# Performance work log

Measured on AMD Instinct MI355X. Metric: run time of the kernel, lower is better.

Reference implementation:

```python
import jax, jax.numpy as jnp
import numpy as np

D_EMB = 1024
N_H = 16
D_H = D_EMB // N_H

def setup_inputs() -> dict:
    key = jax.random.key(0)
    ks = jax.random.split(key, 9)
    s = 1.0 / np.sqrt(D_EMB)
    inp = {"x": jax.random.normal(ks[0], (2, 2048, D_EMB), dtype=jnp.float32)}
    for i, name in enumerate(["q", "k", "v", "o"]):
        inp[f"W{name}"] = jax.random.uniform(ks[1 + 2 * i], (D_EMB, D_EMB), minval=-s, maxval=s, dtype=jnp.float32)
        inp[f"b{name}"] = jax.random.uniform(ks[2 + 2 * i], (D_EMB,), minval=-s, maxval=s, dtype=jnp.float32)
    return inp

def reference(x, Wq, bq, Wk, bk, Wv, bv, Wo, bo):
    B, S, D = x.shape
    # torch Linear: y = x @ W.T + b
    Q = x @ Wq.T + bq
    K = x @ Wk.T + bk
    V = x @ Wv.T + bv
    # [B, H, S, d_h]
    Qh = Q.reshape(B, S, N_H, D_H).transpose(0, 2, 1, 3)
    Kh = K.reshape(B, S, N_H, D_H).transpose(0, 2, 1, 3)
    Vh = V.reshape(B, S, N_H, D_H).transpose(0, 2, 1, 3)
    scores = jnp.einsum("bhsd,bhtd->bhst", Qh, Kh) / jnp.sqrt(jnp.float32(D_H))
    causal = jnp.tril(jnp.ones((S, S), dtype=bool))
    scores = jnp.where(causal, scores, -jnp.inf)
    attn = jax.nn.softmax(scores, axis=-1)
    out = jnp.einsum("bhst,bhtd->bhsd", attn, Vh)
    out = out.transpose(0, 2, 1, 3).reshape(B, S, D)
    return out @ Wo.T + bo
```

## Files before the change

kernel.cpp:

```cpp
#include <hip/hip_runtime.h>
#include <stdint.h>

#define B_  2
#define S_  2048
#define D_  1024
#define H_  16
#define DH_ 64
#define M_  (B_ * S_)

#define NEG_BIG   (-1.0e30f)
#define EXP_FLOOR (-60.0f)
#define FIXED_M   16.0f

typedef uint16_t u16;
typedef uint32_t u32;
typedef u16   u16x4  __attribute__((ext_vector_type(4)));
typedef u16   u16x8  __attribute__((ext_vector_type(8)));
typedef u32   u32x4  __attribute__((ext_vector_type(4)));
typedef __bf16 bf16_t;
typedef bf16_t bf16x8 __attribute__((ext_vector_type(8)));
typedef float floatx4 __attribute__((ext_vector_type(4)));

__device__ __forceinline__ u16 f2b(float f) {
  u32 u = __float_as_uint(f);
  return (u16)((u + 0x7FFFu + ((u >> 16) & 1u)) >> 16);
}
__device__ __forceinline__ u16x8 tr8(const float* p) {
  u16x8 lo = *(const u16x8*)p;
  u16x8 hi = *(const u16x8*)(p + 4);
  return __builtin_shufflevector(lo, hi, 1, 3, 5, 7, 9, 11, 13, 15);
}
__device__ __forceinline__ bf16x8 bc8(u16x8 v) { return __builtin_bit_cast(bf16x8, v); }

__global__ __launch_bounds__(256) void qkv_kernel(
    const float* __restrict__ X,
    const float* __restrict__ Wq, const float* __restrict__ Wk, const float* __restrict__ Wv,
    const float* __restrict__ bq, const float* __restrict__ bk, const float* __restrict__ bv,
    u16* __restrict__ Qb, u16* __restrict__ Kb, u16* __restrict__ Vb)
{
  const int which = blockIdx.y >> 3;
  const float* W    = (which == 0) ? Wq : (which == 1) ? Wk : Wv;
  const float* bias = (which == 0) ? bq : (which == 1) ? bk : bv;
  u16* Y            = (which == 0) ? Qb : (which == 1) ? Kb : Vb;
  const int gm = blockIdx.x * 128;
  const int gn = (blockIdx.y & 7) * 128;

  __shared__ u16 Xl[128][40];
  __shared__ u16 Wl[128][40];

  const int t    = threadIdx.x;
  const int srow = t >> 1;
  const int scol = (t & 1) * 16;
  const int wave = t >> 6;
  const int lane = t & 63;
  const int wm = (wave >> 1) * 64, wn = (wave & 1) * 64;
  const int c = lane & 15, g = lane >> 4;

  const float* xsrc = X + (size_t)(gm + srow) * D_ + scol;
  const float* wsrc = W + (size_t)(gn + srow) * D_ + scol;

  u16x8 xr0 = tr8(xsrc), xr1 = tr8(xsrc + 8);
  u16x8 wr0 = tr8(wsrc), wr1 = tr8(wsrc + 8);

  floatx4 acc[4][4] = {};

  for (int kb = 0; kb < D_; kb += 32) {
    __syncthreads();
    *(u16x8*)&Xl[srow][scol]     = xr0;
    *(u16x8*)&Xl[srow][scol + 8] = xr1;
    *(u16x8*)&Wl[srow][scol]     = wr0;
    *(u16x8*)&Wl[srow][scol + 8] = wr1;
    __syncthreads();

    if (kb + 32 < D_) {
      xr0 = tr8(xsrc + kb + 32); xr1 = tr8(xsrc + kb + 40);
      wr0 = tr8(wsrc + kb + 32); wr1 = tr8(wsrc + kb + 40);
    }

    bf16x8 am[4], bn[4];
#pragma unroll
    for (int i = 0; i < 4; ++i) {
      am[i] = bc8(*(const u16x8*)&Xl[wm + 16 * i + c][8 * g]);
      bn[i] = bc8(*(const u16x8*)&Wl[wn + 16 * i + c][8 * g]);
    }
#pragma unroll
    for (int mi = 0; mi < 4; ++mi)
#pragma unroll
      for (int ni = 0; ni < 4; ++ni)
        acc[mi][ni] = __builtin_amdgcn_mfma_f32_16x16x32_bf16(am[mi], bn[ni], acc[mi][ni], 0, 0, 0);
  }

#pragma unroll
  for (int ni = 0; ni < 4; ++ni) {
    const int col = gn + wn + 16 * ni + c;
    const float bv_ = bias[col];
#pragma unroll
    for (int mi = 0; mi < 4; ++mi)
#pragma unroll
      for (int r = 0; r < 4; ++r)
        Y[(size_t)(gm + wm + 16 * mi + 4 * g + r) * D_ + col] = f2b(acc[mi][ni][r] + bv_);
  }
}

__global__ __launch_bounds__(256) void proj_kernel(
    const u16* __restrict__ A, const float* __restrict__ W,
    const float* __restrict__ bias, float* __restrict__ Y)
{
  const int gm = blockIdx.x * 128;
  const int gn = blockIdx.y * 64;

  __shared__ u16 Al[128][40];
  __shared__ u16 Wl[64][40];

  const int t = threadIdx.x;
  const int wave = t >> 6, lane = t & 63;
  const int wm = (wave >> 1) * 64, wn = (wave & 1) * 32;
  const int c = lane & 15, g = lane >> 4;
  const int ar_ = t >> 1, ac_ = (t & 1) * 16;
  const int wr_ = t >> 2, wc_ = (t & 3) * 8;

  const u16*   asrc = A + (size_t)(gm + ar_) * D_ + ac_;
  const float* wsrc = W + (size_t)(gn + wr_) * D_ + wc_;

  u16x8 a0 = *(const u16x8*)asrc;
  u16x8 a1 = *(const u16x8*)(asrc + 8);
  u16x8 w0 = tr8(wsrc);

  floatx4 acc[4][2] = {};

  for (int kb = 0; kb < D_; kb += 32) {
    __syncthreads();
    *(u16x8*)&Al[ar_][ac_]     = a0;
    *(u16x8*)&Al[ar_][ac_ + 8] = a1;
    *(u16x8*)&Wl[wr_][wc_]     = w0;
    __syncthreads();

    if (kb + 32 < D_) {
      a0 = *(const u16x8*)(asrc + kb + 32);
      a1 = *(const u16x8*)(asrc + kb + 40);
      w0 = tr8(wsrc + kb + 32);
    }

    bf16x8 am[4], bn[2];
#pragma unroll
    for (int i = 0; i < 4; ++i) am[i] = bc8(*(const u16x8*)&Al[wm + 16 * i + c][8 * g]);
#pragma unroll
    for (int i = 0; i < 2; ++i) bn[i] = bc8(*(const u16x8*)&Wl[wn + 16 * i + c][8 * g]);
#pragma unroll
    for (int mi = 0; mi < 4; ++mi)
#pragma unroll
      for (int ni = 0; ni < 2; ++ni)
        acc[mi][ni] = __builtin_amdgcn_mfma_f32_16x16x32_bf16(am[mi], bn[ni], acc[mi][ni], 0, 0, 0);
  }

#pragma unroll
  for (int ni = 0; ni < 2; ++ni) {
    const int col = gn + wn + 16 * ni + c;
    const float bv_ = bias[col];
#pragma unroll
    for (int mi = 0; mi < 4; ++mi)
#pragma unroll
      for (int r = 0; r < 4; ++r)
        Y[(size_t)(gm + wm + 16 * mi + 4 * g + r) * D_ + col] = acc[mi][ni][r] + bv_;
  }
}

__global__ __launch_bounds__(256) void attn_kernel(
    const u16* __restrict__ Qg, const u16* __restrict__ Kg,
    const u16* __restrict__ Vg, u16* __restrict__ Og)
{
  const int bh = blockIdx.x;
  const int b = bh >> 4, h = bh & 15;
  const int qb = 31 - blockIdx.y;
  const int q0 = qb * 64;

  __shared__ u16 Kl[64][72];
  __shared__ u16 Vt[64][72];

  const int t = threadIdx.x;
  const int wave = t >> 6, lane = t & 63;
  const int c = lane & 15, g = lane >> 4;
  const int qrow = q0 + wave * 16 + c;

  bf16x8 qf[2];
  {
    const u16* qsrc = Qg + (size_t)(b * S_ + qrow) * D_ + h * DH_ + 8 * g;
    qf[0] = bc8(*(const u16x8*)qsrc);
    qf[1] = bc8(*(const u16x8*)(qsrc + 32));
  }

  float l_run = 0.f;
  floatx4 o[4] = {};

  const int kr = t >> 2, kc = (t & 3) * 16;
  const int vkp = t & 31, vdg = t >> 5;

  u16x8 kreg0, kreg1;
  u32 vpack[8];
  {
    const u16* ksrc = Kg + (size_t)(b * S_ + kr) * D_ + h * DH_ + kc;
    kreg0 = *(const u16x8*)ksrc;
    kreg1 = *(const u16x8*)(ksrc + 8);
    const u16* vsrc = Vg + (size_t)(b * S_ + 2 * vkp) * D_ + h * DH_ + 8 * vdg;
    u16x8 va = *(const u16x8*)vsrc;
    u16x8 vb2 = *(const u16x8*)(vsrc + D_);
#pragma unroll
    for (int i = 0; i < 8; ++i) vpack[i] = (u32)va[i] | ((u32)vb2[i] << 16);
  }

  for (int kt = 0; kt <= qb; ++kt) {
    const int k0 = kt * 64;
    __syncthreads();
    *(u16x8*)&Kl[kr][kc]     = kreg0;
    *(u16x8*)&Kl[kr][kc + 8] = kreg1;
#pragma unroll
    for (int i = 0; i < 8; ++i) *(u32*)&Vt[8 * vdg + i][2 * vkp] = vpack[i];
    __syncthreads();

    if (kt < qb) {
      const u16* ksrc = Kg + (size_t)(b * S_ + k0 + 64 + kr) * D_ + h * DH_ + kc;
      kreg0 = *(const u16x8*)ksrc;
      kreg1 = *(const u16x8*)(ksrc + 8);
      const u16* vsrc = Vg + (size_t)(b * S_ + k0 + 64 + 2 * vkp) * D_ + h * DH_ + 8 * vdg;
      u16x8 va = *(const u16x8*)vsrc;
      u16x8 vb2 = *(const u16x8*)(vsrc + D_);
#pragma unroll
      for (int i = 0; i < 8; ++i) vpack[i] = (u32)va[i] | ((u32)vb2[i] << 16);
    }

    floatx4 st[4] = {};
#pragma unroll
    for (int mb = 0; mb < 4; ++mb) {
      bf16x8 a0 = bc8(*(const u16x8*)&Kl[16 * mb + c][8 * g]);
      bf16x8 a1 = bc8(*(const u16x8*)&Kl[16 * mb + c][32 + 8 * g]);
      st[mb] = __builtin_amdgcn_mfma_f32_16x16x32_bf16(a0, qf[0], st[mb], 0, 0, 0);
      st[mb] = __builtin_amdgcn_mfma_f32_16x16x32_bf16(a1, qf[1], st[mb], 0, 0, 0);
    }

    u32 plo[4], phi[4];
    float psum = 0.f;
    const bool diag = (kt == qb);
#pragma unroll
    for (int mb = 0; mb < 4; ++mb) {
      u32 pb[4];
#pragma unroll
      for (int r = 0; r < 4; ++r) {
        float arg = fmaf(st[mb][r], 0.125f, -FIXED_M);
        if (diag && (k0 + 16 * mb + 4 * g + r > qrow)) arg = NEG_BIG;
        arg = fmaxf(arg, EXP_FLOOR);
        float p = __expf(arg);
        pb[r] = __float_as_uint(p) & 0xFFFF0000u;
        psum += __uint_as_float(pb[r]);
      }
      plo[mb] = (pb[0] >> 16) | pb[1];
      phi[mb] = (pb[2] >> 16) | pb[3];
    }
    l_run += psum;

    const int s1 = c + 32 * (g & 1);
    const int s2 = s1 + 16;
    const bool hi = (g >= 2);
#pragma unroll
    for (int ks = 0; ks < 2; ++ks) {
      u32 q0a = (u32)__shfl((int)plo[2 * ks],     s1);
      u32 q1a = (u32)__shfl((int)phi[2 * ks],     s1);
      u32 q2a = (u32)__shfl((int)plo[2 * ks],     s2);
      u32 q3a = (u32)__shfl((int)phi[2 * ks],     s2);
      u32 q0b = (u32)__shfl((int)plo[2 * ks + 1], s1);
      u32 q1b = (u32)__shfl((int)phi[2 * ks + 1], s1);
      u32 q2b = (u32)__shfl((int)plo[2 * ks + 1], s2);
      u32 q3b = (u32)__shfl((int)phi[2 * ks + 1], s2);
      u32x4 pa = { hi ? q0b : q0a, hi ? q1b : q1a, hi ? q2b : q2a, hi ? q3b : q3a };
      bf16x8 pfrag = __builtin_bit_cast(bf16x8, pa);
#pragma unroll
      for (int nb = 0; nb < 4; ++nb) {
        bf16x8 vf = bc8(*(const u16x8*)&Vt[16 * nb + c][32 * ks + 8 * g]);
        o[nb] = __builtin_amdgcn_mfma_f32_16x16x32_bf16(vf, pfrag, o[nb], 0, 0, 0);
      }
    }
  }

  l_run += __shfl_xor(l_run, 16);
  l_run += __shfl_xor(l_run, 32);
  const float inv = 1.0f / l_run;
#pragma unroll
  for (int nb = 0; nb < 4; ++nb) {
    u16x4 ov;
#pragma unroll
    for (int r = 0; r < 4; ++r) ov[r] = f2b(o[nb][r] * inv);
    *(u16x4*)(Og + (size_t)(b * S_ + qrow) * D_ + h * DH_ + 16 * nb + 4 * g) = ov;
  }
}

extern "C" void kernel_launch(void* const* d_in, const int* in_sizes, int n_in,
                              void* d_out, int out_size, void* d_ws, size_t ws_size,
                              hipStream_t stream) {
  const float* x  = (const float*)d_in[0];
  const float* Wq = (const float*)d_in[1];
  const float* bq = (const float*)d_in[2];
  const float* Wk = (const float*)d_in[3];
  const float* bk = (const float*)d_in[4];
  const float* Wv = (const float*)d_in[5];
  const float* bv = (const float*)d_in[6];
  const float* Wo = (const float*)d_in[7];
  const float* bo = (const float*)d_in[8];

  u16* Qb = (u16*)d_ws;
  u16* Vb = (u16*)d_out;
  u16* Kb = Vb + (size_t)M_ * D_;

  qkv_kernel<<<dim3(32, 24), 256, 0, stream>>>(x, Wq, Wk, Wv, bq, bk, bv, Qb, Kb, Vb);
  attn_kernel<<<dim3(B_ * H_, 32), 256, 0, stream>>>(Qb, Kb, Vb, Qb);
  proj_kernel<<<dim3(32, 16), 256, 0, stream>>>(Qb, Wo, bo, (float*)d_out);
}
```

Measured before the change: 216.9 us.

## Pre-convert inputs to bf16 and stream GEMM tiles via async global-to-LDS loads

Adds a conversion kernel that turns x and all four weight matrices to bf16 in workspace once per call. The QKV and output-projection GEMMs then load bf16 tiles straight into double-buffered, XOR-swizzled LDS using global_load_lds, replacing register staging and the fp32-to-bf16 shuffle. The projection tile shape also changes from 128x64 to 64x128. This adds an extra kernel launch and extra memory traffic for the conversion pass. The pipeline keeps only one barrier per k-step, which may be fragile.

Result: faster. 194.0 us (-10.5%).

```diff
diff --git a/kernel.cpp b/kernel.cpp
--- a/kernel.cpp
+++ b/kernel.cpp
@@ -25,63 +25,92 @@
   u32 u = __float_as_uint(f);
   return (u16)((u + 0x7FFFu + ((u >> 16) & 1u)) >> 16);
 }
-__device__ __forceinline__ u16x8 tr8(const float* p) {
-  u16x8 lo = *(const u16x8*)p;
-  u16x8 hi = *(const u16x8*)(p + 4);
-  return __builtin_shufflevector(lo, hi, 1, 3, 5, 7, 9, 11, 13, 15);
-}
 __device__ __forceinline__ bf16x8 bc8(u16x8 v) { return __builtin_bit_cast(bf16x8, v); }
 
+__device__ __forceinline__ void async16(u16* lds, const u16* g) {
+  __builtin_amdgcn_global_load_lds(
+      (const __attribute__((address_space(1))) u32*)g,
+      (__attribute__((address_space(3))) u32*)lds, 16, 0, 0);
+}
+
+__global__ __launch_bounds__(256) void cvt_kernel(
+    const float* __restrict__ X,
+    const float* __restrict__ Wq, const float* __restrict__ Wk,
+    const float* __restrict__ Wv, const float* __restrict__ Wo,
+    u16* __restrict__ Xb, u16* __restrict__ Wqb, u16* __restrict__ Wkb,
+    u16* __restrict__ Wvb, u16* __restrict__ Wob)
+{
+  const int XC = (M_ * D_) / 8;
+  const int WC = (D_ * D_) / 8;
+  const int total = XC + 4 * WC;
+  for (int cid = blockIdx.x * 256 + threadIdx.x; cid < total; cid += gridDim.x * 256) {
+    const float* src; u16* dst; int off;
+    if (cid < XC)               { src = X;  dst = Xb;  off = cid; }
+    else if (cid < XC + WC)     { src = Wq; dst = Wqb; off = cid - XC; }
+    else if (cid < XC + 2 * WC) { src = Wk; dst = Wkb; off = cid - XC - WC; }
+    else if (cid < XC + 3 * WC) { src = Wv; dst = Wvb; off = cid - XC - 2 * WC; }
+    else                        { src = Wo; dst = Wob; off = cid - XC - 3 * WC; }
+    const float4* p = (const float4*)(src + (size_t)off * 8);
+    float4 lo = p[0], hi = p[1];
+    u16x8 o;
+    o[0] = f2b(lo.x); o[1] = f2b(lo.y); o[2] = f2b(lo.z); o[3] = f2b(lo.w);
+    o[4] = f2b(hi.x); o[5] = f2b(hi.y); o[6] = f2b(hi.z); o[7] = f2b(hi.w);
+    *(u16x8*)(dst + (size_t)off * 8) = o;
+  }
+}
+
 __global__ __launch_bounds__(256) void qkv_kernel(
-    const float* __restrict__ X,
-    const float* __restrict__ Wq, const float* __restrict__ Wk, const float* __restrict__ Wv,
+    const u16* __restrict__ Xb,
+    const u16* __restrict__ Wqb, const u16* __restrict__ Wkb, const u16* __restrict__ Wvb,
     const float* __restrict__ bq, const float* __restrict__ bk, const float* __restrict__ bv,
     u16* __restrict__ Qb, u16* __restrict__ Kb, u16* __restrict__ Vb)
 {
   const int which = blockIdx.y >> 3;
-  const float* W    = (which == 0) ? Wq : (which == 1) ? Wk : Wv;
+  const u16* W      = (which == 0) ? Wqb : (which == 1) ? Wkb : Wvb;
   const float* bias = (which == 0) ? bq : (which == 1) ? bk : bv;
   u16* Y            = (which == 0) ? Qb : (which == 1) ? Kb : Vb;
   const int gm = blockIdx.x * 128;
   const int gn = (blockIdx.y & 7) * 128;
 
-  __shared__ u16 Xl[128][40];
-  __shared__ u16 Wl[128][40];
-
-  const int t    = threadIdx.x;
-  const int srow = t >> 1;
-  const int scol = (t & 1) * 16;
-  const int wave = t >> 6;
-  const int lane = t & 63;
-  const int wm = (wave >> 1) * 64, wn = (wave & 1) * 64;
-  const int c = lane & 15, g = lane >> 4;
-
-  const float* xsrc = X + (size_t)(gm + srow) * D_ + scol;
-  const float* wsrc = W + (size_t)(gn + srow) * D_ + scol;
-
-  u16x8 xr0 = tr8(xsrc), xr1 = tr8(xsrc + 8);
-  u16x8 wr0 = tr8(wsrc), wr1 = tr8(wsrc + 8);
+  __shared__ u16 Al[2][128][32];
+  __shared__ u16 Bl[2][128][32];
+
+  const int t  = threadIdx.x;
+  const int wv = t >> 6, ln = t & 63;
+  const int c  = ln & 15, g = ln >> 4;
+  const int wm = (wv >> 1) * 64, wn = (wv & 1) * 64;
+
+  const int srow   = ln >> 2;
+  const int schunk = (ln & 3) ^ ((ln >> 3) & 3);
+  const u16* a0 = Xb + (size_t)(gm + wv * 16 + srow) * D_ + schunk * 8;
+  const u16* a1 = a0 + (size_t)64 * D_;
+  const u16* b0 = W  + (size_t)(gn + wv * 16 + srow) * D_ + schunk * 8;
+  const u16* b1 = b0 + (size_t)64 * D_;
 
   floatx4 acc[4][4] = {};
-
-  for (int kb = 0; kb < D_; kb += 32) {
+  const int rsw = (c >> 1) & 3;
+
+  async16(&Al[0][wv * 16][0],      a0);
+  async16(&Al[0][64 + wv * 16][0], a1);
+  async16(&Bl[0][wv * 16][0],      b0);
+  async16(&Bl[0][64 + wv * 16][0], b1);
+
+  for (int kt = 0; kt < D_ / 32; ++kt) {
     __syncthreads();
-    *(u16x8*)&Xl[srow][scol]     = xr0;
-    *(u16x8*)&Xl[srow][scol + 8] = xr1;
-    *(u16x8*)&Wl[srow][scol]     = wr0;
-    *(u16x8*)&Wl[srow][scol + 8] = wr1;
-    __syncthreads();
-
-    if (kb + 32 < D_) {
-      xr0 = tr8(xsrc + kb + 32); xr1 = tr8(xsrc + kb + 40);
-      wr0 = tr8(wsrc + kb + 32); wr1 = tr8(wsrc + kb + 40);
-    }
-
+    if (kt + 1 < D_ / 32) {
+      const int nb = (kt + 1) & 1;
+      const int ko = (kt + 1) * 32;
+      async16(&Al[nb][wv * 16][0],      a0 + ko);
+      async16(&Al[nb][64 + wv * 16][0], a1 + ko);
+      async16(&Bl[nb][wv * 16][0],      b0 + ko);
+      async16(&Bl[nb][64 + wv * 16][0], b1 + ko);
+    }
+    const int bf = kt & 1;
     bf16x8 am[4], bn[4];
 #pragma unroll
     for (int i = 0; i < 4; ++i) {
-      am[i] = bc8(*(const u16x8*)&Xl[wm + 16 * i + c][8 * g]);
-      bn[i] = bc8(*(const u16x8*)&Wl[wn + 16 * i + c][8 * g]);
+      am[i] = bc8(*(const u16x8*)&Al[bf][wm + 16 * i + c][(g ^ rsw) * 8]);
+      bn[i] = bc8(*(const u16x8*)&Bl[bf][wn + 16 * i + c][(g ^ rsw) * 8]);
     }
 #pragma unroll
     for (int mi = 0; mi < 4; ++mi)
@@ -103,62 +132,63 @@
 }
 
 __global__ __launch_bounds__(256) void proj_kernel(
-    const u16* __restrict__ A, const float* __restrict__ W,
+    const u16* __restrict__ A, const u16* __restrict__ Wb,
     const float* __restrict__ bias, float* __restrict__ Y)
 {
-  const int gm = blockIdx.x * 128;
-  const int gn = blockIdx.y * 64;
-
-  __shared__ u16 Al[128][40];
-  __shared__ u16 Wl[64][40];
-
-  const int t = threadIdx.x;
-  const int wave = t >> 6, lane = t & 63;
-  const int wm = (wave >> 1) * 64, wn = (wave & 1) * 32;
-  const int c = lane & 15, g = lane >> 4;
-  const int ar_ = t >> 1, ac_ = (t & 1) * 16;
-  const int wr_ = t >> 2, wc_ = (t & 3) * 8;
-
-  const u16*   asrc = A + (size_t)(gm + ar_) * D_ + ac_;
-  const float* wsrc = W + (size_t)(gn + wr_) * D_ + wc_;
-
-  u16x8 a0 = *(const u16x8*)asrc;
-  u16x8 a1 = *(const u16x8*)(asrc + 8);
-  u16x8 w0 = tr8(wsrc);
-
-  floatx4 acc[4][2] = {};
-
-  for (int kb = 0; kb < D_; kb += 32) {
+  const int gm = blockIdx.x * 64;
+  const int gn = blockIdx.y * 128;
+
+  __shared__ u16 Al[2][64][32];
+  __shared__ u16 Bl[2][128][32];
+
+  const int t  = threadIdx.x;
+  const int wv = t >> 6, ln = t & 63;
+  const int c  = ln & 15, g = ln >> 4;
+  const int wm = (wv >> 1) * 32, wn = (wv & 1) * 64;
+
+  const int srow   = ln >> 2;
+  const int schunk = (ln & 3) ^ ((ln >> 3) & 3);
+  const u16* a0 = A  + (size_t)(gm + wv * 16 + srow) * D_ + schunk * 8;
+  const u16* b0 = Wb + (size_t)(gn + wv * 16 + srow) * D_ + schunk * 8;
+  const u16* b1 = b0 + (size_t)64 * D_;
+
+  floatx4 acc[2][4] = {};
+  const int rsw = (c >> 1) & 3;
+
+  async16(&Al[0][wv * 16][0],      a0);
+  async16(&Bl[0][wv * 16][0],      b0);
+  async16(&Bl[0][64 + wv * 16][0], b1);
+
+  for (int kt = 0; kt < D_ / 32; ++kt) {
     __syncthreads();
-    *(u16x8*)&Al[ar_][ac_]     = a0;
-    *(u16x8*)&Al[ar_][ac_ + 8] = a1;
-    *(u16x8*)&Wl[wr_][wc_]     = w0;
-    __syncthreads();
-
-    if (kb + 32 < D_) {
-      a0 = *(const u16x8*)(asrc + kb + 32);
-      a1 = *(const u16x8*)(asrc + kb + 40);
-      w0 = tr8(wsrc + kb + 32);
-    }
-
-    bf16x8 am[4], bn[2];
-#pragma unroll
-    for (int i = 0; i < 4; ++i) am[i] = bc8(*(const u16x8*)&Al[wm + 16 * i + c][8 * g]);
-#pragma unroll
-    for (int i = 0; i < 2; ++i) bn[i] = bc8(*(const u16x8*)&Wl[wn + 16 * i + c][8 * g]);
-#pragma unroll
-    for (int mi = 0; mi < 4; ++mi)
-#pragma unroll
-      for (int ni = 0; ni < 2; ++ni)
+    if (kt + 1 < D_ / 32) {
+      const int nb = (kt + 1) & 1;
+      const int ko = (kt + 1) * 32;
+      async16(&Al[nb][wv * 16][0],      a0 + ko);
+      async16(&Bl[nb][wv * 16][0],      b0 + ko);
+      async16(&Bl[nb][64 + wv * 16][0], b1 + ko);
+    }
+    const int bf = kt & 1;
+    bf16x8 am[2], bn[4];
+#pragma unroll
+    for (int i = 0; i < 2; ++i)
+      am[i] = bc8(*(const u16x8*)&Al[bf][wm + 16 * i + c][(g ^ rsw) * 8]);
+#pragma unroll
+    for (int i = 0; i < 4; ++i)
+      bn[i] = bc8(*(const u16x8*)&Bl[bf][wn + 16 * i + c][(g ^ rsw) * 8]);
+#pragma unroll
+    for (int mi = 0; mi < 2; ++mi)
+#pragma unroll
+      for (int ni = 0; ni < 4; ++ni)
         acc[mi][ni] = __builtin_amdgcn_mfma_f32_16x16x32_bf16(am[mi], bn[ni], acc[mi][ni], 0, 0, 0);
   }
 
 #pragma unroll
-  for (int ni = 0; ni < 2; ++ni) {
+  for (int ni = 0; ni < 4; ++ni) {
     const int col = gn + wn + 16 * ni + c;
     const float bv_ = bias[col];
 #pragma unroll
-    for (int mi = 0; mi < 4; ++mi)
+    for (int mi = 0; mi < 2; ++mi)
 #pragma unroll
       for (int r = 0; r < 4; ++r)
         Y[(size_t)(gm + wm + 16 * mi + 4 * g + r) * D_ + col] = acc[mi][ni][r] + bv_;
@@ -305,11 +335,17 @@
   const float* Wo = (const float*)d_in[7];
   const float* bo = (const float*)d_in[8];
 
-  u16* Qb = (u16*)d_ws;
-  u16* Vb = (u16*)d_out;
-  u16* Kb = Vb + (size_t)M_ * D_;
-
-  qkv_kernel<<<dim3(32, 24), 256, 0, stream>>>(x, Wq, Wk, Wv, bq, bk, bv, Qb, Kb, Vb);
+  u16* Xb  = (u16*)d_ws;
+  u16* Wqb = Xb  + (size_t)M_ * D_;
+  u16* Wkb = Wqb + (size_t)D_ * D_;
+  u16* Wvb = Wkb + (size_t)D_ * D_;
+  u16* Wob = Wvb + (size_t)D_ * D_;
+  u16* Qb  = Wob + (size_t)D_ * D_;
+  u16* Vb  = (u16*)d_out;
+  u16* Kb  = Vb + (size_t)M_ * D_;
+
+  cvt_kernel<<<dim3(2048), 256, 0, stream>>>(x, Wq, Wk, Wv, Wo, Xb, Wqb, Wkb, Wvb, Wob);
+  qkv_kernel<<<dim3(32, 24), 256, 0, stream>>>(Xb, Wqb, Wkb, Wvb, bq, bk, bv, Qb, Kb, Vb);
   attn_kernel<<<dim3(B_ * H_, 32), 256, 0, stream>>>(Qb, Kb, Vb, Qb);
-  proj_kernel<<<dim3(32, 16), 256, 0, stream>>>(Qb, Wo, bo, (float*)d_out);
-}
+  proj_kernel<<<dim3(64, 8), 256, 0, stream>>>(Qb, Wob, bo, (float*)d_out);
+}
```
